# Optimization experiments

Hardware: AMD Instinct MI355X
Metric: run time of the kernel (lower is better)

## Reference

```python
import jax, jax.numpy as jnp
import numpy as np

B, C, H, W = 8, 64, 128, 128
G, DGPG = 4, 1
GD = G * DGPG          # total deformable groups = 4
COUT = 64
KH = KW = 3
K = KH * KW            # 9 kernel locations
PAD = STR = DIL = 1
HO, WO = 128, 128      # same padding, stride 1
OFFSET_SCALE = 1.0
CDG = C // GD          # channels per deformable group = 16
CPG = C // G           # input channels per conv group = 16
KOFF = 7
POFF = 3


def dwconv7(x, w, b):
    # depthwise 7x7 conv, groups == channels; w: [C,1,7,7]
    y = jax.lax.conv_general_dilated(
        x, w, window_strides=(1, 1), padding=[(POFF, POFF), (POFF, POFF)],
        feature_group_count=C, dimension_numbers=('NCHW', 'OIHW', 'NCHW'))
    return y + b[None, :, None, None]


def gn1(x, g, b):
    # GroupNorm with a single group: normalize over (C,H,W) per sample
    m = x.mean(axis=(1, 2, 3), keepdims=True)
    v = x.var(axis=(1, 2, 3), keepdims=True)
    return (x - m) * jax.lax.rsqrt(v + 1e-5) * g[None, :, None, None] + b[None, :, None, None]


def pw(x, w, b):
    # 1x1 conv; w: [O, C]
    return jnp.einsum('bchw,oc->bohw', x, w) + b[None, :, None, None]


def setup_inputs() -> dict:
    key = jax.random.key(0)
    ks = jax.random.split(key, 8)
    s = 0.02
    return {
        'x': jax.random.normal(ks[0], (B, C, H, W), jnp.float32),
        'w_dw_off': jax.random.normal(ks[1], (C, 1, KOFF, KOFF), jnp.float32) * s,
        'b_dw_off': jnp.zeros((C,), jnp.float32),
        'gn_off_g': jnp.ones((C,), jnp.float32),
        'gn_off_b': jnp.zeros((C,), jnp.float32),
        'w_pw_off': jax.random.normal(ks[2], (GD * K * 2, C), jnp.float32) * s,
        'b_pw_off': jnp.zeros((GD * K * 2,), jnp.float32),
        'w_dw_m': jax.random.normal(ks[3], (C, 1, KOFF, KOFF), jnp.float32) * s,
        'b_dw_m': jnp.zeros((C,), jnp.float32),
        'gn_m_g': jnp.ones((C,), jnp.float32),
        'gn_m_b': jnp.zeros((C,), jnp.float32),
        'w_pw_m': jax.random.normal(ks[4], (GD * K, C), jnp.float32) * s,
        'b_pw_m': jnp.zeros((GD * K,), jnp.float32),
        'weight': jax.random.normal(ks[5], (COUT, CPG, KH, KW), jnp.float32) * s,
        'bias': jax.random.normal(ks[6], (COUT,), jnp.float32) * s,
    }


def _deform_conv(x, offset, mask, weight, bias):
    # offset: [B, GD, K, 2, HO, WO] (y, x); mask: [B, GD, K, HO, WO] (softmaxed)
    ky, kx = jnp.meshgrid(jnp.arange(KH), jnp.arange(KW), indexing='ij')
    ky = ky.reshape(K).astype(x.dtype)
    kx = kx.reshape(K).astype(x.dtype)
    oy = jnp.arange(HO, dtype=x.dtype)
    ox = jnp.arange(WO, dtype=x.dtype)
    base_y = oy[None, :] * STR - PAD + ky[:, None] * DIL   # [K, HO]
    base_x = ox[None, :] * STR - PAD + kx[:, None] * DIL   # [K, WO]
    py = base_y[None, None, :, :, None] + offset[:, :, :, 0] * OFFSET_SCALE  # [B,GD,K,HO,WO]
    px = base_x[None, None, :, None, :] + offset[:, :, :, 1] * OFFSET_SCALE

    x_flat = x.reshape(B, GD, CDG, H * W)
    y0 = jnp.floor(py)
    x0 = jnp.floor(px)
    wy = py - y0
    wx = px - x0

    def gather(yi, xi):
        valid = ((yi >= 0) & (yi < H) & (xi >= 0) & (xi < W)).astype(x.dtype)
        yc = jnp.clip(yi, 0, H - 1).astype(jnp.int32)
        xc = jnp.clip(xi, 0, W - 1).astype(jnp.int32)
        idx = (yc * W + xc).reshape(B, GD, 1, K * HO * WO)
        v = jnp.take_along_axis(x_flat, idx, axis=3).reshape(B, GD, CDG, K, HO, WO)
        return v * valid[:, :, None]

    v = (gather(y0, x0) * ((1 - wy) * (1 - wx))[:, :, None]
         + gather(y0, x0 + 1) * ((1 - wy) * wx)[:, :, None]
         + gather(y0 + 1, x0) * (wy * (1 - wx))[:, :, None]
         + gather(y0 + 1, x0 + 1) * (wy * wx)[:, :, None])
    v = v * mask[:, :, None]                               # modulated samples
    v = v.reshape(B, G, CPG, K, HO, WO)
    wg = weight.reshape(G, COUT // G, CPG, K)
    out = jnp.einsum('bgckhw,gock->bgohw', v, wg).reshape(B, COUT, HO, WO)
    return out + bias[None, :, None, None]


def reference(x, w_dw_off, b_dw_off, gn_off_g, gn_off_b, w_pw_off, b_pw_off,
              w_dw_m, b_dw_m, gn_m_g, gn_m_b, w_pw_m, b_pw_m, weight, bias):
    off = pw(gn1(dwconv7(x, w_dw_off, b_dw_off), gn_off_g, gn_off_b), w_pw_off, b_pw_off)
    m = pw(gn1(dwconv7(x, w_dw_m, b_dw_m), gn_m_g, gn_m_b), w_pw_m, b_pw_m)
    offset = off.reshape(B, GD, K, 2, HO, WO)
    mask = jax.nn.softmax(m.reshape(B, GD, K, HO, WO), axis=2)  # attn over kernel points
    return _deform_conv(x, offset, mask, weight, bias)
```

## Files before the change

kernel.cpp:

```cpp
#include <hip/hip_runtime.h>
#include <hip/hip_fp16.h>
#include <math.h>

#define HW     16384
#define IMG_H  128
#define IMG_W  128

typedef _Float16 f16x2 __attribute__((ext_vector_type(2)));
typedef __fp16 fp16v2 __attribute__((ext_vector_type(2)));
typedef _Float16 f16x4 __attribute__((ext_vector_type(4)));
typedef float f32x4 __attribute__((ext_vector_type(4)));

#define OFF_T2    ((size_t)0)
#define OFF_XT    ((size_t)8388608)
#define OFF_WT    ((size_t)12582912)
#define OFF_PART  ((size_t)12599040)
#define OFF_AD    ((size_t)12631808)
#define OFF_WB    ((size_t)19711744)
#define OFF_WDW2  ((size_t)19716352)
#define OFF_WBO   ((size_t)19719936)
#define OFF_WBM   ((size_t)19752704)
#define OFF_DC    ((size_t)19769088)

__global__ void k_prep(const float* __restrict__ wpw_off,
                       const float* __restrict__ wpw_m,
                       const float* __restrict__ wdef,
                       const float* __restrict__ wdwo,
                       const float* __restrict__ wdwm,
                       float* __restrict__ ws) {
    int i = blockIdx.x * 256 + threadIdx.x;
    if (i < 6912) {
        int c = i / 108, o = i % 108;
        ws[OFF_WT + i] = (o < 72) ? wpw_off[o * 64 + c] : wpw_m[(o - 72) * 64 + c];
    } else if (i < 9216) {
        int j = i - 6912;
        int lane = j & 63;
        int gt = j >> 6;
        int tap = gt % 9, g = gt / 9;
        int oc = lane & 15, qh = lane >> 4;
        union { ushort h[4]; uint2 u; } pk;
#pragma unroll
        for (int jj = 0; jj < 4; ++jj) {
            float wv = wdef[((g * 16 + oc) * 16 + (4 * qh + jj)) * 9 + tap];
            pk.h[jj] = __half_as_ushort(__float2half(wv));
        }
        ((uint2*)(ws + OFF_WB))[j] = pk.u;
    } else if (i < 12800) {
        int j = i - 9216;
        int q = j & 3;
        int r = j >> 2;
        int dy = r % 7;
        int cv = (r / 7) & 1;
        int c = r / 14;
        const float* src = cv ? wdwm : wdwo;
        int dx0 = q * 2;
        float w0 = src[c * 49 + dy * 7 + dx0];
        float w1 = (dx0 + 1 < 7) ? src[c * 49 + dy * 7 + dx0 + 1] : 0.f;
        union { __half h[2]; uint u; } pk;
        pk.h[0] = __float2half(w0);
        pk.h[1] = __float2half(w1);
        ((uint*)(ws + OFF_WDW2))[j] = pk.u;
    }
}

__global__ __launch_bounds__(256) void k_trans(const float* __restrict__ x,
                                               __half* __restrict__ xT) {
    int n = blockIdx.x * 256 + threadIdx.x;
    int p = n & (HW - 1);
    int bg = n >> 14;
    const float* src = x + (size_t)bg * 16 * HW + p;
    union { __half2 h2[8]; uint4 u[2]; } pk;
#pragma unroll
    for (int i = 0; i < 8; ++i) {
        float a = src[(size_t)(2 * i) * HW];
        float bq = src[(size_t)(2 * i + 1) * HW];
        pk.h2[i] = __halves2half2(__float2half(a), __float2half(bq));
    }
    uint4* dst = (uint4*)(xT + (size_t)n * 16);
    dst[0] = pk.u[0];
    dst[1] = pk.u[1];
}

__global__ __launch_bounds__(256) void k_dw(const float* __restrict__ x,
                                            const float* __restrict__ bdwo,
                                            const float* __restrict__ bdwm,
                                            const uint* __restrict__ wdw2,
                                            uint2* __restrict__ t2p,
                                            float* __restrict__ partial) {
    int bid = blockIdx.x;
    int b = bid >> 9;
    int c2 = (bid >> 4) & 31;
    int stripe = (bid & 15) * 8;
    int t = threadIdx.x;
    int cb = t & 31;
    int row = stripe + (t >> 5);
    int c0 = c2 * 2;

    float vo[2][4], vm[2][4];
    float s1o = 0.f, s2o = 0.f, s1m = 0.f, s2m = 0.f;
    union CV { fp16v2 v; f16x2 h; };
    union WU { uint u; f16x2 h; };

#pragma unroll
    for (int ch = 0; ch < 2; ++ch) {
        int c = c0 + ch;
        const float4* pl = (const float4*)(x + ((size_t)(b * 64 + c)) * HW);
        const uint* wp = wdw2 + c * 56;
        float acco[4] = {0.f, 0.f, 0.f, 0.f};
        float accm[4] = {0.f, 0.f, 0.f, 0.f};
#pragma unroll
        for (int dy = 0; dy < 7; ++dy) {
            int iy = row - 3 + dy;
            if (iy >= 0 && iy < IMG_H) {
                const float4* prow = pl + iy * 32;
                float4 f4 = prow[cb];
                float4 f4m = prow[cb == 0 ? 0 : cb - 1];
                float4 f4p = prow[cb == 31 ? 31 : cb + 1];
                bool le = (cb == 0), re = (cb == 31);
                float v[11];
                v[0] = le ? 0.f : f4m.y;
                v[1] = le ? 0.f : f4m.z;
                v[2] = le ? 0.f : f4m.w;
                v[3] = f4.x; v[4] = f4.y; v[5] = f4.z; v[6] = f4.w;
                v[7] = re ? 0.f : f4p.x;
                v[8] = re ? 0.f : f4p.y;
                v[9] = re ? 0.f : f4p.z;
                v[10] = re ? 0.f : f4p.w;
                f16x2 hp[10];
#pragma unroll
                for (int d = 0; d < 10; ++d) {
                    CV cv;
                    cv.v = __builtin_amdgcn_cvt_pkrtz(v[d], v[d + 1]);
                    hp[d] = cv.h;
                }
#pragma unroll
                for (int cc = 0; cc < 4; ++cc) {
                    WU w0, w1, w2, w3, u0, u1, u2, u3;
                    w0.u = wp[dy * 4 + 0]; w1.u = wp[dy * 4 + 1];
                    w2.u = wp[dy * 4 + 2]; w3.u = wp[dy * 4 + 3];
                    u0.u = wp[28 + dy * 4 + 0]; u1.u = wp[28 + dy * 4 + 1];
                    u2.u = wp[28 + dy * 4 + 2]; u3.u = wp[28 + dy * 4 + 3];
                    float ao = acco[cc], am = accm[cc];
                    ao = __builtin_amdgcn_fdot2(hp[cc],     w0.h, ao, false);
                    ao = __builtin_amdgcn_fdot2(hp[cc + 2], w1.h, ao, false);
                    ao = __builtin_amdgcn_fdot2(hp[cc + 4], w2.h, ao, false);
                    ao = __builtin_amdgcn_fdot2(hp[cc + 6], w3.h, ao, false);
                    am = __builtin_amdgcn_fdot2(hp[cc],     u0.h, am, false);
                    am = __builtin_amdgcn_fdot2(hp[cc + 2], u1.h, am, false);
                    am = __builtin_amdgcn_fdot2(hp[cc + 4], u2.h, am, false);
                    am = __builtin_amdgcn_fdot2(hp[cc + 6], u3.h, am, false);
                    acco[cc] = ao; accm[cc] = am;
                }
            }
        }
        float bo = bdwo[c], bm = bdwm[c];
#pragma unroll
        for (int cc = 0; cc < 4; ++cc) {
            float o_ = acco[cc] + bo, m_ = accm[cc] + bm;
            vo[ch][cc] = o_; vm[ch][cc] = m_;
            s1o += o_; s2o += o_ * o_; s1m += m_; s2m += m_ * m_;
        }
    }

    union { uint2 u2[4]; uint4 u4[2]; } ot;
#pragma unroll
    for (int cc = 0; cc < 4; ++cc) {
        ot.u2[cc].x = (uint)__half_as_ushort(__float2half(vo[0][cc])) |
                      ((uint)__half_as_ushort(__float2half(vo[1][cc])) << 16);
        ot.u2[cc].y = (uint)__half_as_ushort(__float2half(vm[0][cc])) |
                      ((uint)__half_as_ushort(__float2half(vm[1][cc])) << 16);
    }
    uint4* dst = (uint4*)(t2p + ((size_t)(b * 32 + c2) * HW + row * IMG_W + cb * 4));
    dst[0] = ot.u4[0];
    dst[1] = ot.u4[1];

#pragma unroll
    for (int d = 32; d; d >>= 1) {
        s1o += __shfl_down(s1o, d);
        s2o += __shfl_down(s2o, d);
        s1m += __shfl_down(s1m, d);
        s2m += __shfl_down(s2m, d);
    }
    __shared__ float red[4][4];
    if ((t & 63) == 0) {
        int w = t >> 6;
        red[w][0] = s1o; red[w][1] = s2o; red[w][2] = s1m; red[w][3] = s2m;
    }
    __syncthreads();
    if (t < 4) {
        float v = red[0][t] + red[1][t] + red[2][t] + red[3][t];
        partial[(size_t)bid * 4 + t] = v;
    }
}

__global__ __launch_bounds__(256) void k_fin(const float* __restrict__ partial,
                      const float* __restrict__ gog, const float* __restrict__ gob,
                      const float* __restrict__ gmg, const float* __restrict__ gmb,
                      float* __restrict__ ad) {
    int b = blockIdx.x, t = threadIdx.x;
    const float4* pp = (const float4*)partial + (size_t)b * 512;
    float4 s = make_float4(0.f, 0.f, 0.f, 0.f);
#pragma unroll
    for (int i = 0; i < 2; ++i) {
        float4 v = pp[t + i * 256];
        s.x += v.x; s.y += v.y; s.z += v.z; s.w += v.w;
    }
#pragma unroll
    for (int d = 32; d; d >>= 1) {
        s.x += __shfl_down(s.x, d);
        s.y += __shfl_down(s.y, d);
        s.z += __shfl_down(s.z, d);
        s.w += __shfl_down(s.w, d);
    }
    __shared__ float red[4][4];
    if ((t & 63) == 0) {
        int w = t >> 6;
        red[w][0] = s.x; red[w][1] = s.y; red[w][2] = s.z; red[w][3] = s.w;
    }
    __syncthreads();
    if (t < 64) {
        float s1o = red[0][0] + red[1][0] + red[2][0] + red[3][0];
        float s2o = red[0][1] + red[1][1] + red[2][1] + red[3][1];
        float s1m = red[0][2] + red[1][2] + red[2][2] + red[3][2];
        float s2m = red[0][3] + red[1][3] + red[2][3] + red[3][3];
        int c = t;
        const float invN = 1.f / 1048576.f;
        float m_o = s1o * invN;
        float v_o = s2o * invN - m_o * m_o;
        float i_o = rsqrtf(v_o + 1e-5f);
        float m_m = s1m * invN;
        float v_m = s2m * invN - m_m * m_m;
        float i_m = rsqrtf(v_m + 1e-5f);
        float a_o = i_o * gog[c];
        float d_o = gob[c] - m_o * a_o;
        float a_m = i_m * gmg[c];
        float d_m = gmb[c] - m_m * a_m;
        ((float4*)ad)[b * 64 + c] = make_float4(a_o, d_o, a_m, d_m);
    }
}

__global__ __launch_bounds__(256) void k_fold(const float* __restrict__ wT,
                                              const float* __restrict__ ad,
                                              const float* __restrict__ bpo,
                                              const float* __restrict__ bpm,
                                              uint2* __restrict__ wbo,
                                              uint2* __restrict__ wbm,
                                              float* __restrict__ dconst) {
    int b = blockIdx.x, t = threadIdx.x;
    const float* adb = ad + b * 256;
    for (int i = t; i < 2048; i += 256) {
        int lane = i & 63;
        int f = i >> 6;
        int g = f >> 3, kk = (f >> 1) & 3, nf = f & 1;
        int n = lane & 15, q = lane >> 4;
        int out = nf * 16 + n;
        union { ushort h[4]; uint2 u; } pk;
#pragma unroll
        for (int jj = 0; jj < 4; ++jj) {
            int ch = kk * 16 + 4 * q + jj;
            float w = (out < 18) ? adb[ch * 4 + 0] * wT[ch * 108 + g * 18 + out] : 0.f;
            pk.h[jj] = __half_as_ushort(__float2half(w));
        }
        wbo[((size_t)(b * 4) + g) * 8 * 64 + (size_t)(kk * 2 + nf) * 64 + lane] = pk.u;
    }
    for (int i = t; i < 1024; i += 256) {
        int lane = i & 63;
        int f = i >> 6;
        int g = f >> 2, kk = f & 3;
        int n = lane & 15, q = lane >> 4;
        union { ushort h[4]; uint2 u; } pk;
#pragma unroll
        for (int jj = 0; jj < 4; ++jj) {
            int ch = kk * 16 + 4 * q + jj;
            float w = (n < 9) ? adb[ch * 4 + 2] * wT[ch * 108 + 72 + g * 9 + n] : 0.f;
            pk.h[jj] = __half_as_ushort(__float2half(w));
        }
        wbm[((size_t)(b * 4) + g) * 4 * 64 + (size_t)kk * 64 + lane] = pk.u;
    }
    if (t < 108) {
        float s = (t < 72) ? bpo[t] : bpm[t - 72];
        for (int c = 0; c < 64; ++c) {
            float d = (t < 72) ? adb[c * 4 + 1] : adb[c * 4 + 3];
            s = fmaf(d, wT[c * 108 + t], s);
        }
        dconst[b * 108 + t] = s;
    }
}

__global__ __launch_bounds__(256, 4) void k_gthf(const uint2* __restrict__ t2p,
                                                 const uint2* __restrict__ wbo,
                                                 const uint2* __restrict__ wbm,
                                                 const float* __restrict__ dconst,
                                                 const __half* __restrict__ xT,
                                                 const uint2* __restrict__ wb,
                                                 const float* __restrict__ bias,
                                                 float* __restrict__ out) {
    __shared__ union SMem {
        struct {
            uint4 xsA[506];
            uint4 xsB[506];
            uint  slab[5120];
        } s;
        float shout[4864];
    } sm;

    int tid = threadIdx.x;
    int bid = blockIdx.x;
    int bg = bid >> 6;
    int tile = bid & 63;
    int tr = tile >> 3, tc = tile & 7;
    int r0 = tr * 16, c0 = tc * 16;
    int g = bg & 3, b = bg >> 2;
    int wr0 = r0 - 3, wc0 = c0 - 3;

    const __half* xg = xT + (size_t)bg * HW * 16;

#pragma unroll
    for (int it = 0; it < 2; ++it) {
        int idx = tid + it * 256;
        if (idx < 484) {
            int ly = idx / 22, lx = idx - ly * 22;
            int sr = wr0 + ly; sr = sr < 0 ? 0 : (sr > 127 ? 127 : sr);
            int sc = wc0 + lx; sc = sc < 0 ? 0 : (sc > 127 ? 127 : sc);
            const uint4* src = (const uint4*)(xg + (size_t)(sr * IMG_W + sc) * 16);
            sm.s.xsA[ly * 23 + lx] = src[0];
            sm.s.xsB[ly * 23 + lx] = src[1];
        }
    }

    int row = r0 + (tid >> 4), col = c0 + (tid & 15);
    int p = row * IMG_W + col;
    int lane = tid & 63, wv = tid >> 6;
    int m_idx = lane & 15, q_idx = lane >> 4;

    union BU { uint2 u; f16x4 h; };

    const uint2* wboP = wbo + ((size_t)(b * 4) + g) * 8 * 64 + lane;
    const uint2* wbmP = wbm + ((size_t)(b * 4) + g) * 4 * 64 + lane;
    f16x4 bO[8], bM[4];
#pragma unroll
    for (int i = 0; i < 8; ++i) { BU t; t.u = wboP[i * 64]; bO[i] = t.h; }
#pragma unroll
    for (int i = 0; i < 4; ++i) { BU t; t.u = wbmP[i * 64]; bM[i] = t.h; }

    const uint2* wbp = wb + (size_t)(g * 9) * 64 + lane;
    f16x4 bfr[9];
#pragma unroll
    for (int k = 0; k < 9; ++k) { BU t; t.u = wbp[k * 64]; bfr[k] = t.h; }

    uint* aslab = sm.s.slab + wv * 1280;
    const uint2* tp = t2p + (size_t)b * 32 * HW + p;

    f32x4 accO0[4], accO1[4], accM[4];
#pragma unroll
    for (int s = 0; s < 4; ++s) {
        accO0[s] = (f32x4){0.f, 0.f, 0.f, 0.f};
        accO1[s] = (f32x4){0.f, 0.f, 0.f, 0.f};
        accM[s]  = (f32x4){0.f, 0.f, 0.f, 0.f};
    }

#pragma unroll
    for (int kk = 0; kk < 4; ++kk) {
        uint2 v[8];
#pragma unroll
        for (int j = 0; j < 8; ++j) v[j] = tp[(size_t)(kk * 8 + j) * HW];
        uint* rowp = aslab + lane * 20;
        ((uint4*)rowp)[0] = make_uint4(v[0].x, v[1].x, v[2].x, v[3].x);
        ((uint4*)rowp)[1] = make_uint4(v[4].x, v[5].x, v[6].x, v[7].x);
        ((uint4*)(rowp + 8))[0] = make_uint4(v[0].y, v[1].y, v[2].y, v[3].y);
        ((uint4*)(rowp + 8))[1] = make_uint4(v[4].y, v[5].y, v[6].y, v[7].y);
#pragma unroll
        for (int s = 0; s < 4; ++s) {
            const uint* pr = aslab + (s * 16 + m_idx) * 20 + 2 * q_idx;
            BU ao, am;
            ao.u = *(const uint2*)pr;
            am.u = *(const uint2*)(pr + 8);
            accO0[s] = __builtin_amdgcn_mfma_f32_16x16x16f16(ao.h, bO[kk * 2 + 0], accO0[s], 0, 0, 0);
            accO1[s] = __builtin_amdgcn_mfma_f32_16x16x16f16(ao.h, bO[kk * 2 + 1], accO1[s], 0, 0, 0);
            accM[s]  = __builtin_amdgcn_mfma_f32_16x16x16f16(am.h, bM[kk], accM[s], 0, 0, 0);
        }
    }

    const float* dc = dconst + b * 108;

#pragma unroll
    for (int s = 0; s < 4; ++s)
#pragma unroll
        for (int j = 0; j < 4; ++j) {
            int px = s * 16 + 4 * q_idx + j;
            union { __half2 h2; uint u; } pk;
            pk.h2 = __halves2half2(__float2half(accO0[s][j]),
                                   __float2half(accO1[s][j]));
            aslab[px * 20 + m_idx] = pk.u;
        }
    float facc[18];
    {
        const uint4* dr = (const uint4*)(aslab + lane * 20);
        uint4 d0 = dr[0], d1 = dr[1], d2 = dr[2], d3 = dr[3];
        uint du[16] = {d0.x, d0.y, d0.z, d0.w, d1.x, d1.y, d1.z, d1.w,
                       d2.x, d2.y, d2.z, d2.w, d3.x, d3.y, d3.z, d3.w};
        union { uint u; __half2 h2; } cv;
#pragma unroll
        for (int i = 0; i < 16; ++i) {
            cv.u = du[i];
            float2 f = __half22float2(cv.h2);
            facc[i] = f.x + dc[g * 18 + i];
            if (i < 2) facc[16 + i] = f.y + dc[g * 18 + 16 + i];
        }
    }

    {
        float* fsl = (float*)aslab;
#pragma unroll
        for (int s = 0; s < 4; ++s)
#pragma unroll
            for (int j = 0; j < 4; ++j) {
                int px = s * 16 + 4 * q_idx + j;
                fsl[px * 20 + m_idx] = accM[s][j];
            }
        float macc[9];
#pragma unroll
        for (int k = 0; k < 9; ++k) macc[k] = fsl[lane * 20 + k] + dc[72 + g * 9 + k];
        float mx = macc[0];
#pragma unroll
        for (int k = 1; k < 9; ++k) mx = fmaxf(mx, macc[k]);
        float ssum = 0.f;
#pragma unroll
        for (int k = 0; k < 9; ++k) {
            float e = __expf(macc[k] - mx);
            macc[k] = e;
            ssum += e;
        }
        float inv = 1.f / ssum;
#pragma unroll
        for (int k = 0; k < 9; ++k) facc[k] = facc[k], macc[k] *= inv;

        __syncthreads();

        uint4* shvw = (uint4*)aslab + lane * 3;
        const _Float16* shvh = (const _Float16*)aslab;

        f32x4 acc[4];
#pragma unroll
        for (int s = 0; s < 4; ++s) acc[s] = (f32x4){0.f, 0.f, 0.f, 0.f};

#pragma unroll
        for (int k = 0; k < 9; ++k) {
            float mk = macc[k];
            float py = (float)(row + k / 3 - 1) + facc[k * 2 + 0];
            float px = (float)(col + k % 3 - 1) + facc[k * 2 + 1];
            float y0f = floorf(py), x0f = floorf(px);
            float wy = py - y0f, wx = px - x0f;
            int iy0 = (int)y0f, ix0 = (int)x0f;
            int iy1 = iy0 + 1, ix1 = ix0 + 1;
            float fy0 = (iy0 >= 0 && iy0 < IMG_H) ? (1.f - wy) : 0.f;
            float fy1 = (iy1 >= 0 && iy1 < IMG_H) ? wy : 0.f;
            float fx0 = (ix0 >= 0 && ix0 < IMG_W) ? (1.f - wx) : 0.f;
            float fx1 = (ix1 >= 0 && ix1 < IMG_W) ? wx : 0.f;
            __half2 f00h = __float2half2_rn(fy0 * fx0 * mk);
            __half2 f01h = __float2half2_rn(fy0 * fx1 * mk);
            __half2 f10h = __float2half2_rn(fy1 * fx0 * mk);
            __half2 f11h = __float2half2_rn(fy1 * fx1 * mk);
            int ly0 = iy0 - wr0; ly0 = ly0 < 0 ? 0 : (ly0 > 21 ? 21 : ly0);
            int ly1 = iy1 - wr0; ly1 = ly1 < 0 ? 0 : (ly1 > 21 ? 21 : ly1);
            int lx0 = ix0 - wc0; lx0 = lx0 < 0 ? 0 : (lx0 > 21 ? 21 : lx0);
            int lx1 = ix1 - wc0; lx1 = lx1 < 0 ? 0 : (lx1 > 21 ? 21 : lx1);
            int i00 = ly0 * 23 + lx0, i01 = ly0 * 23 + lx1;
            int i10 = ly1 * 23 + lx0, i11 = ly1 * 23 + lx1;
            union Q8 { uint4 u[2]; __half2 h2[8]; };
            Q8 q00, q01, q10, q11;
            q00.u[0] = sm.s.xsA[i00]; q00.u[1] = sm.s.xsB[i00];
            q01.u[0] = sm.s.xsA[i01]; q01.u[1] = sm.s.xsB[i01];
            q10.u[0] = sm.s.xsA[i10]; q10.u[1] = sm.s.xsB[i10];
            q11.u[0] = sm.s.xsA[i11]; q11.u[1] = sm.s.xsB[i11];
            union V8 { __half2 h2[4]; uint4 u; };
            V8 pa, pb;
#pragma unroll
            for (int i = 0; i < 4; ++i) {
                __half2 vh = __hmul2(f00h, q00.h2[i]);
                vh = __hfma2(f01h, q01.h2[i], vh);
                vh = __hfma2(f10h, q10.h2[i], vh);
                vh = __hfma2(f11h, q11.h2[i], vh);
                pa.h2[i] = vh;
            }
#pragma unroll
            for (int i = 4; i < 8; ++i) {
                __half2 vh = __hmul2(f00h, q00.h2[i]);
                vh = __hfma2(f01h, q01.h2[i], vh);
                vh = __hfma2(f10h, q10.h2[i], vh);
                vh = __hfma2(f11h, q11.h2[i], vh);
                pb.h2[i - 4] = vh;
            }
            shvw[0] = pa.u;
            shvw[1] = pb.u;
#pragma unroll
            for (int s = 0; s < 4; ++s) {
                f16x4 af = *(const f16x4*)(shvh +
                            ((size_t)(s * 16 + m_idx)) * 24 + q_idx * 4);
                acc[s] = __builtin_amdgcn_mfma_f32_16x16x16f16(af, bfr[k], acc[s], 0, 0, 0);
            }
        }

        __syncthreads();

#pragma unroll
        for (int s = 0; s < 4; ++s)
#pragma unroll
            for (int j = 0; j < 4; ++j)
                sm.shout[(wv * 64 + s * 16 + 4 * q_idx + j) * 19 + m_idx] = acc[s][j];

        float* outp = out + ((size_t)b * 64 + g * 16) * HW + p;
#pragma unroll
        for (int o = 0; o < 16; ++o)
            outp[(size_t)o * HW] = sm.shout[tid * 19 + o] + bias[g * 16 + o];
    }
}

extern "C" void kernel_launch(void* const* d_in, const int* in_sizes, int n_in,
                              void* d_out, int out_size, void* d_ws, size_t ws_size,
                              hipStream_t stream) {
    const float* x        = (const float*)d_in[0];
    const float* w_dw_off = (const float*)d_in[1];
    const float* b_dw_off = (const float*)d_in[2];
    const float* gn_off_g = (const float*)d_in[3];
    const float* gn_off_b = (const float*)d_in[4];
    const float* w_pw_off = (const float*)d_in[5];
    const float* b_pw_off = (const float*)d_in[6];
    const float* w_dw_m   = (const float*)d_in[7];
    const float* b_dw_m   = (const float*)d_in[8];
    const float* gn_m_g   = (const float*)d_in[9];
    const float* gn_m_b   = (const float*)d_in[10];
    const float* w_pw_m   = (const float*)d_in[11];
    const float* b_pw_m   = (const float*)d_in[12];
    const float* weight   = (const float*)d_in[13];
    const float* bias     = (const float*)d_in[14];

    float* ws = (float*)d_ws;
    uint2* t2p    = (uint2*)(ws + OFF_T2);
    __half* xT    = (__half*)(ws + OFF_XT);
    float* wT     = ws + OFF_WT;
    float* part   = ws + OFF_PART;
    float* adb    = ws + OFF_AD;
    const uint2* wb = (const uint2*)(ws + OFF_WB);
    const uint* wdw2 = (const uint*)(ws + OFF_WDW2);
    uint2* wbo    = (uint2*)(ws + OFF_WBO);
    uint2* wbm    = (uint2*)(ws + OFF_WBM);
    float* dconst = ws + OFF_DC;

    k_prep<<<50, 256, 0, stream>>>(w_pw_off, w_pw_m, weight, w_dw_off, w_dw_m, ws);
    k_trans<<<2048, 256, 0, stream>>>(x, xT);
    k_dw<<<4096, 256, 0, stream>>>(x, b_dw_off, b_dw_m, wdw2, t2p, part);
    k_fin<<<8, 256, 0, stream>>>(part, gn_off_g, gn_off_b, gn_m_g, gn_m_b, adb);
    k_fold<<<8, 256, 0, stream>>>(wT, adb, b_pw_off, b_pw_m, wbo, wbm, dconst);
    k_gthf<<<2048, 256, 0, stream>>>(t2p, wbo, wbm, dconst, xT, wb, bias, (float*)d_out);
}
```

Before: 100.7 us.

## Fuse GN finalize with weight folding and software-pipeline loads in gather kernel

Merges the GroupNorm finalize and weight-fold kernels into one launch that keeps the per-channel scale and shift in shared memory, removing a launch and a global round trip. In the main gather kernel, the x-tile loads are held in registers and written to shared memory only after the offset/mask MFMA stage, so their latency overlaps that compute. The t2p feature loads are double-buffered across kk iterations, and the deform-conv weight fragment loads are moved later in the kernel. Holding more values in registers raises register pressure, which may reduce occupancy under the 256x4 launch bounds.

```diff
diff --git a/kernel.cpp b/kernel.cpp
--- a/kernel.cpp
+++ b/kernel.cpp
@@ -15,7 +15,6 @@
 #define OFF_XT    ((size_t)8388608)
 #define OFF_WT    ((size_t)12582912)
 #define OFF_PART  ((size_t)12599040)
-#define OFF_AD    ((size_t)12631808)
 #define OFF_WB    ((size_t)19711744)
 #define OFF_WDW2  ((size_t)19716352)
 #define OFF_WBO   ((size_t)19719936)
@@ -193,61 +192,58 @@
     }
 }
 
-__global__ __launch_bounds__(256) void k_fin(const float* __restrict__ partial,
+__global__ __launch_bounds__(256) void k_finfold(const float* __restrict__ partial,
                       const float* __restrict__ gog, const float* __restrict__ gob,
                       const float* __restrict__ gmg, const float* __restrict__ gmb,
-                      float* __restrict__ ad) {
+                      const float* __restrict__ wT,
+                      const float* __restrict__ bpo,
+                      const float* __restrict__ bpm,
+                      uint2* __restrict__ wbo,
+                      uint2* __restrict__ wbm,
+                      float* __restrict__ dconst) {
+    __shared__ float adsh[256];
     int b = blockIdx.x, t = threadIdx.x;
-    const float4* pp = (const float4*)partial + (size_t)b * 512;
-    float4 s = make_float4(0.f, 0.f, 0.f, 0.f);
-#pragma unroll
-    for (int i = 0; i < 2; ++i) {
-        float4 v = pp[t + i * 256];
-        s.x += v.x; s.y += v.y; s.z += v.z; s.w += v.w;
-    }
-#pragma unroll
-    for (int d = 32; d; d >>= 1) {
-        s.x += __shfl_down(s.x, d);
-        s.y += __shfl_down(s.y, d);
-        s.z += __shfl_down(s.z, d);
-        s.w += __shfl_down(s.w, d);
-    }
-    __shared__ float red[4][4];
-    if ((t & 63) == 0) {
-        int w = t >> 6;
-        red[w][0] = s.x; red[w][1] = s.y; red[w][2] = s.z; red[w][3] = s.w;
-    }
-    __syncthreads();
-    if (t < 64) {
-        float s1o = red[0][0] + red[1][0] + red[2][0] + red[3][0];
-        float s2o = red[0][1] + red[1][1] + red[2][1] + red[3][1];
-        float s1m = red[0][2] + red[1][2] + red[2][2] + red[3][2];
-        float s2m = red[0][3] + red[1][3] + red[2][3] + red[3][3];
-        int c = t;
-        const float invN = 1.f / 1048576.f;
-        float m_o = s1o * invN;
-        float v_o = s2o * invN - m_o * m_o;
-        float i_o = rsqrtf(v_o + 1e-5f);
-        float m_m = s1m * invN;
-        float v_m = s2m * invN - m_m * m_m;
-        float i_m = rsqrtf(v_m + 1e-5f);
-        float a_o = i_o * gog[c];
-        float d_o = gob[c] - m_o * a_o;
-        float a_m = i_m * gmg[c];
-        float d_m = gmb[c] - m_m * a_m;
-        ((float4*)ad)[b * 64 + c] = make_float4(a_o, d_o, a_m, d_m);
-    }
-}
-
-__global__ __launch_bounds__(256) void k_fold(const float* __restrict__ wT,
-                                              const float* __restrict__ ad,
-                                              const float* __restrict__ bpo,
-                                              const float* __restrict__ bpm,
-                                              uint2* __restrict__ wbo,
-                                              uint2* __restrict__ wbm,
-                                              float* __restrict__ dconst) {
-    int b = blockIdx.x, t = threadIdx.x;
-    const float* adb = ad + b * 256;
+    {
+        const float4* pp = (const float4*)partial + (size_t)b * 512;
+        float4 s = make_float4(0.f, 0.f, 0.f, 0.f);
+#pragma unroll
+        for (int i = 0; i < 2; ++i) {
+            float4 v = pp[t + i * 256];
+            s.x += v.x; s.y += v.y; s.z += v.z; s.w += v.w;
+        }
+#pragma unroll
+        for (int d = 32; d; d >>= 1) {
+            s.x += __shfl_down(s.x, d);
+            s.y += __shfl_down(s.y, d);
+            s.z += __shfl_down(s.z, d);
+            s.w += __shfl_down(s.w, d);
+        }
+        __shared__ float red[4][4];
+        if ((t & 63) == 0) {
+            int w = t >> 6;
+            red[w][0] = s.x; red[w][1] = s.y; red[w][2] = s.z; red[w][3] = s.w;
+        }
+        __syncthreads();
+        if (t < 64) {
+            float s1o = red[0][0] + red[1][0] + red[2][0] + red[3][0];
+            float s2o = red[0][1] + red[1][1] + red[2][1] + red[3][1];
+            float s1m = red[0][2] + red[1][2] + red[2][2] + red[3][2];
+            float s2m = red[0][3] + red[1][3] + red[2][3] + red[3][3];
+            int c = t;
+            const float invN = 1.f / 1048576.f;
+            float m_o = s1o * invN;
+            float v_o = s2o * invN - m_o * m_o;
+            float i_o = rsqrtf(v_o + 1e-5f);
+            float m_m = s1m * invN;
+            float v_m = s2m * invN - m_m * m_m;
+            float i_m = rsqrtf(v_m + 1e-5f);
+            adsh[c * 4 + 0] = i_o * gog[c];
+            adsh[c * 4 + 1] = gob[c] - m_o * (i_o * gog[c]);
+            adsh[c * 4 + 2] = i_m * gmg[c];
+            adsh[c * 4 + 3] = gmb[c] - m_m * (i_m * gmg[c]);
+        }
+        __syncthreads();
+    }
     for (int i = t; i < 2048; i += 256) {
         int lane = i & 63;
         int f = i >> 6;
@@ -258,7 +254,7 @@
 #pragma unroll
         for (int jj = 0; jj < 4; ++jj) {
             int ch = kk * 16 + 4 * q + jj;
-            float w = (out < 18) ? adb[ch * 4 + 0] * wT[ch * 108 + g * 18 + out] : 0.f;
+            float w = (out < 18) ? adsh[ch * 4 + 0] * wT[ch * 108 + g * 18 + out] : 0.f;
             pk.h[jj] = __half_as_ushort(__float2half(w));
         }
         wbo[((size_t)(b * 4) + g) * 8 * 64 + (size_t)(kk * 2 + nf) * 64 + lane] = pk.u;
@@ -272,7 +268,7 @@
 #pragma unroll
         for (int jj = 0; jj < 4; ++jj) {
             int ch = kk * 16 + 4 * q + jj;
-            float w = (n < 9) ? adb[ch * 4 + 2] * wT[ch * 108 + 72 + g * 9 + n] : 0.f;
+            float w = (n < 9) ? adsh[ch * 4 + 2] * wT[ch * 108 + 72 + g * 9 + n] : 0.f;
             pk.h[jj] = __half_as_ushort(__float2half(w));
         }
         wbm[((size_t)(b * 4) + g) * 4 * 64 + (size_t)kk * 64 + lane] = pk.u;
@@ -280,7 +276,7 @@
     if (t < 108) {
         float s = (t < 72) ? bpo[t] : bpm[t - 72];
         for (int c = 0; c < 64; ++c) {
-            float d = (t < 72) ? adb[c * 4 + 1] : adb[c * 4 + 3];
+            float d = (t < 72) ? adsh[c * 4 + 1] : adsh[c * 4 + 3];
             s = fmaf(d, wT[c * 108 + t], s);
         }
         dconst[b * 108 + t] = s;
@@ -315,16 +311,20 @@
 
     const __half* xg = xT + (size_t)bg * HW * 16;
 
+    int sidx[2];
+    uint4 sA[2], sB[2];
 #pragma unroll
     for (int it = 0; it < 2; ++it) {
         int idx = tid + it * 256;
+        sidx[it] = -1;
         if (idx < 484) {
             int ly = idx / 22, lx = idx - ly * 22;
             int sr = wr0 + ly; sr = sr < 0 ? 0 : (sr > 127 ? 127 : sr);
             int sc = wc0 + lx; sc = sc < 0 ? 0 : (sc > 127 ? 127 : sc);
             const uint4* src = (const uint4*)(xg + (size_t)(sr * IMG_W + sc) * 16);
-            sm.s.xsA[ly * 23 + lx] = src[0];
-            sm.s.xsB[ly * 23 + lx] = src[1];
+            sA[it] = src[0];
+            sB[it] = src[1];
+            sidx[it] = ly * 23 + lx;
         }
     }
 
@@ -343,11 +343,6 @@
 #pragma unroll
     for (int i = 0; i < 4; ++i) { BU t; t.u = wbmP[i * 64]; bM[i] = t.h; }
 
-    const uint2* wbp = wb + (size_t)(g * 9) * 64 + lane;
-    f16x4 bfr[9];
-#pragma unroll
-    for (int k = 0; k < 9; ++k) { BU t; t.u = wbp[k * 64]; bfr[k] = t.h; }
-
     uint* aslab = sm.s.slab + wv * 1280;
     const uint2* tp = t2p + (size_t)b * 32 * HW + p;
 
@@ -359,16 +354,21 @@
         accM[s]  = (f32x4){0.f, 0.f, 0.f, 0.f};
     }
 
+    uint2 cur[8], nxt[8];
+#pragma unroll
+    for (int j = 0; j < 8; ++j) cur[j] = tp[(size_t)j * HW];
+
 #pragma unroll
     for (int kk = 0; kk < 4; ++kk) {
-        uint2 v[8];
-#pragma unroll
-        for (int j = 0; j < 8; ++j) v[j] = tp[(size_t)(kk * 8 + j) * HW];
+        if (kk < 3) {
+#pragma unroll
+            for (int j = 0; j < 8; ++j) nxt[j] = tp[(size_t)((kk + 1) * 8 + j) * HW];
+        }
         uint* rowp = aslab + lane * 20;
-        ((uint4*)rowp)[0] = make_uint4(v[0].x, v[1].x, v[2].x, v[3].x);
-        ((uint4*)rowp)[1] = make_uint4(v[4].x, v[5].x, v[6].x, v[7].x);
-        ((uint4*)(rowp + 8))[0] = make_uint4(v[0].y, v[1].y, v[2].y, v[3].y);
-        ((uint4*)(rowp + 8))[1] = make_uint4(v[4].y, v[5].y, v[6].y, v[7].y);
+        ((uint4*)rowp)[0] = make_uint4(cur[0].x, cur[1].x, cur[2].x, cur[3].x);
+        ((uint4*)rowp)[1] = make_uint4(cur[4].x, cur[5].x, cur[6].x, cur[7].x);
+        ((uint4*)(rowp + 8))[0] = make_uint4(cur[0].y, cur[1].y, cur[2].y, cur[3].y);
+        ((uint4*)(rowp + 8))[1] = make_uint4(cur[4].y, cur[5].y, cur[6].y, cur[7].y);
 #pragma unroll
         for (int s = 0; s < 4; ++s) {
             const uint* pr = aslab + (s * 16 + m_idx) * 20 + 2 * q_idx;
@@ -379,7 +379,16 @@
             accO1[s] = __builtin_amdgcn_mfma_f32_16x16x16f16(ao.h, bO[kk * 2 + 1], accO1[s], 0, 0, 0);
             accM[s]  = __builtin_amdgcn_mfma_f32_16x16x16f16(am.h, bM[kk], accM[s], 0, 0, 0);
         }
-    }
+#pragma unroll
+        for (int j = 0; j < 8; ++j) cur[j] = nxt[j];
+    }
+
+#pragma unroll
+    for (int it = 0; it < 2; ++it)
+        if (sidx[it] >= 0) {
+            sm.s.xsA[sidx[it]] = sA[it];
+            sm.s.xsB[sidx[it]] = sB[it];
+        }
 
     const float* dc = dconst + b * 108;
 
@@ -409,6 +418,7 @@
         }
     }
 
+    float macc[9];
     {
         float* fsl = (float*)aslab;
 #pragma unroll
@@ -418,7 +428,6 @@
                 int px = s * 16 + 4 * q_idx + j;
                 fsl[px * 20 + m_idx] = accM[s][j];
             }
-        float macc[9];
 #pragma unroll
         for (int k = 0; k < 9; ++k) macc[k] = fsl[lane * 20 + k] + dc[72 + g * 9 + k];
         float mx = macc[0];
@@ -433,87 +442,92 @@
         }
         float inv = 1.f / ssum;
 #pragma unroll
-        for (int k = 0; k < 9; ++k) facc[k] = facc[k], macc[k] *= inv;
-
-        __syncthreads();
-
-        uint4* shvw = (uint4*)aslab + lane * 3;
-        const _Float16* shvh = (const _Float16*)aslab;
-
-        f32x4 acc[4];
-#pragma unroll
-        for (int s = 0; s < 4; ++s) acc[s] = (f32x4){0.f, 0.f, 0.f, 0.f};
-
-#pragma unroll
-        for (int k = 0; k < 9; ++k) {
-            float mk = macc[k];
-            float py = (float)(row + k / 3 - 1) + facc[k * 2 + 0];
-            float px = (float)(col + k % 3 - 1) + facc[k * 2 + 1];
-            float y0f = floorf(py), x0f = floorf(px);
-            float wy = py - y0f, wx = px - x0f;
-            int iy0 = (int)y0f, ix0 = (int)x0f;
-            int iy1 = iy0 + 1, ix1 = ix0 + 1;
-            float fy0 = (iy0 >= 0 && iy0 < IMG_H) ? (1.f - wy) : 0.f;
-            float fy1 = (iy1 >= 0 && iy1 < IMG_H) ? wy : 0.f;
-            float fx0 = (ix0 >= 0 && ix0 < IMG_W) ? (1.f - wx) : 0.f;
-            float fx1 = (ix1 >= 0 && ix1 < IMG_W) ? wx : 0.f;
-            __half2 f00h = __float2half2_rn(fy0 * fx0 * mk);
-            __half2 f01h = __float2half2_rn(fy0 * fx1 * mk);
-            __half2 f10h = __float2half2_rn(fy1 * fx0 * mk);
-            __half2 f11h = __float2half2_rn(fy1 * fx1 * mk);
-            int ly0 = iy0 - wr0; ly0 = ly0 < 0 ? 0 : (ly0 > 21 ? 21 : ly0);
-            int ly1 = iy1 - wr0; ly1 = ly1 < 0 ? 0 : (ly1 > 21 ? 21 : ly1);
-            int lx0 = ix0 - wc0; lx0 = lx0 < 0 ? 0 : (lx0 > 21 ? 21 : lx0);
-            int lx1 = ix1 - wc0; lx1 = lx1 < 0 ? 0 : (lx1 > 21 ? 21 : lx1);
-            int i00 = ly0 * 23 + lx0, i01 = ly0 * 23 + lx1;
-            int i10 = ly1 * 23 + lx0, i11 = ly1 * 23 + lx1;
-            union Q8 { uint4 u[2]; __half2 h2[8]; };
-            Q8 q00, q01, q10, q11;
-            q00.u[0] = sm.s.xsA[i00]; q00.u[1] = sm.s.xsB[i00];
-            q01.u[0] = sm.s.xsA[i01]; q01.u[1] = sm.s.xsB[i01];
-            q10.u[0] = sm.s.xsA[i10]; q10.u[1] = sm.s.xsB[i10];
-            q11.u[0] = sm.s.xsA[i11]; q11.u[1] = sm.s.xsB[i11];
-            union V8 { __half2 h2[4]; uint4 u; };
-            V8 pa, pb;
-#pragma unroll
-            for (int i = 0; i < 4; ++i) {
-                __half2 vh = __hmul2(f00h, q00.h2[i]);
-                vh = __hfma2(f01h, q01.h2[i], vh);
-                vh = __hfma2(f10h, q10.h2[i], vh);
-                vh = __hfma2(f11h, q11.h2[i], vh);
-                pa.h2[i] = vh;
-            }
-#pragma unroll
-            for (int i = 4; i < 8; ++i) {
-                __half2 vh = __hmul2(f00h, q00.h2[i]);
-                vh = __hfma2(f01h, q01.h2[i], vh);
-                vh = __hfma2(f10h, q10.h2[i], vh);
-                vh = __hfma2(f11h, q11.h2[i], vh);
-                pb.h2[i - 4] = vh;
-            }
-            shvw[0] = pa.u;
-            shvw[1] = pb.u;
-#pragma unroll
-            for (int s = 0; s < 4; ++s) {
-                f16x4 af = *(const f16x4*)(shvh +
-                            ((size_t)(s * 16 + m_idx)) * 24 + q_idx * 4);
-                acc[s] = __builtin_amdgcn_mfma_f32_16x16x16f16(af, bfr[k], acc[s], 0, 0, 0);
-            }
-        }
-
-        __syncthreads();
-
-#pragma unroll
-        for (int s = 0; s < 4; ++s)
-#pragma unroll
-            for (int j = 0; j < 4; ++j)
-                sm.shout[(wv * 64 + s * 16 + 4 * q_idx + j) * 19 + m_idx] = acc[s][j];
-
-        float* outp = out + ((size_t)b * 64 + g * 16) * HW + p;
-#pragma unroll
-        for (int o = 0; o < 16; ++o)
-            outp[(size_t)o * HW] = sm.shout[tid * 19 + o] + bias[g * 16 + o];
-    }
+        for (int k = 0; k < 9; ++k) macc[k] *= inv;
+    }
+
+    const uint2* wbp = wb + (size_t)(g * 9) * 64 + lane;
+    f16x4 bfr[9];
+#pragma unroll
+    for (int k = 0; k < 9; ++k) { BU t; t.u = wbp[k * 64]; bfr[k] = t.h; }
+
+    __syncthreads();
+
+    uint4* shvw = (uint4*)aslab + lane * 3;
+    const _Float16* shvh = (const _Float16*)aslab;
+
+    f32x4 acc[4];
+#pragma unroll
+    for (int s = 0; s < 4; ++s) acc[s] = (f32x4){0.f, 0.f, 0.f, 0.f};
+
+#pragma unroll
+    for (int k = 0; k < 9; ++k) {
+        float mk = macc[k];
+        float py = (float)(row + k / 3 - 1) + facc[k * 2 + 0];
+        float px = (float)(col + k % 3 - 1) + facc[k * 2 + 1];
+        float y0f = floorf(py), x0f = floorf(px);
+        float wy = py - y0f, wx = px - x0f;
+        int iy0 = (int)y0f, ix0 = (int)x0f;
+        int iy1 = iy0 + 1, ix1 = ix0 + 1;
+        float fy0 = (iy0 >= 0 && iy0 < IMG_H) ? (1.f - wy) : 0.f;
+        float fy1 = (iy1 >= 0 && iy1 < IMG_H) ? wy : 0.f;
+        float fx0 = (ix0 >= 0 && ix0 < IMG_W) ? (1.f - wx) : 0.f;
+        float fx1 = (ix1 >= 0 && ix1 < IMG_W) ? wx : 0.f;
+        __half2 f00h = __float2half2_rn(fy0 * fx0 * mk);
+        __half2 f01h = __float2half2_rn(fy0 * fx1 * mk);
+        __half2 f10h = __float2half2_rn(fy1 * fx0 * mk);
+        __half2 f11h = __float2half2_rn(fy1 * fx1 * mk);
+        int ly0 = iy0 - wr0; ly0 = ly0 < 0 ? 0 : (ly0 > 21 ? 21 : ly0);
+        int ly1 = iy1 - wr0; ly1 = ly1 < 0 ? 0 : (ly1 > 21 ? 21 : ly1);
+        int lx0 = ix0 - wc0; lx0 = lx0 < 0 ? 0 : (lx0 > 21 ? 21 : lx0);
+        int lx1 = ix1 - wc0; lx1 = lx1 < 0 ? 0 : (lx1 > 21 ? 21 : lx1);
+        int i00 = ly0 * 23 + lx0, i01 = ly0 * 23 + lx1;
+        int i10 = ly1 * 23 + lx0, i11 = ly1 * 23 + lx1;
+        union Q8 { uint4 u[2]; __half2 h2[8]; };
+        Q8 q00, q01, q10, q11;
+        q00.u[0] = sm.s.xsA[i00]; q00.u[1] = sm.s.xsB[i00];
+        q01.u[0] = sm.s.xsA[i01]; q01.u[1] = sm.s.xsB[i01];
+        q10.u[0] = sm.s.xsA[i10]; q10.u[1] = sm.s.xsB[i10];
+        q11.u[0] = sm.s.xsA[i11]; q11.u[1] = sm.s.xsB[i11];
+        union V8 { __half2 h2[4]; uint4 u; };
+        V8 pa, pb;
+#pragma unroll
+        for (int i = 0; i < 4; ++i) {
+            __half2 vh = __hmul2(f00h, q00.h2[i]);
+            vh = __hfma2(f01h, q01.h2[i], vh);
+            vh = __hfma2(f10h, q10.h2[i], vh);
+            vh = __hfma2(f11h, q11.h2[i], vh);
+            pa.h2[i] = vh;
+        }
+#pragma unroll
+        for (int i = 4; i < 8; ++i) {
+            __half2 vh = __hmul2(f00h, q00.h2[i]);
+            vh = __hfma2(f01h, q01.h2[i], vh);
+            vh = __hfma2(f10h, q10.h2[i], vh);
+            vh = __hfma2(f11h, q11.h2[i], vh);
+            pb.h2[i - 4] = vh;
+        }
+        shvw[0] = pa.u;
+        shvw[1] = pb.u;
+#pragma unroll
+        for (int s = 0; s < 4; ++s) {
+            f16x4 af = *(const f16x4*)(shvh +
+                        ((size_t)(s * 16 + m_idx)) * 24 + q_idx * 4);
+            acc[s] = __builtin_amdgcn_mfma_f32_16x16x16f16(af, bfr[k], acc[s], 0, 0, 0);
+        }
+    }
+
+    __syncthreads();
+
+#pragma unroll
+    for (int s = 0; s < 4; ++s)
+#pragma unroll
+        for (int j = 0; j < 4; ++j)
+            sm.shout[(wv * 64 + s * 16 + 4 * q_idx + j) * 19 + m_idx] = acc[s][j];
+
+    float* outp = out + ((size_t)b * 64 + g * 16) * HW + p;
+#pragma unroll
+    for (int o = 0; o < 16; ++o)
+        outp[(size_t)o * HW] = sm.shout[tid * 19 + o] + bias[g * 16 + o];
 }
 
 extern "C" void kernel_launch(void* const* d_in, const int* in_sizes, int n_in,
@@ -540,7 +554,6 @@
     __half* xT    = (__half*)(ws + OFF_XT);
     float* wT     = ws + OFF_WT;
     float* part   = ws + OFF_PART;
-    float* adb    = ws + OFF_AD;
     const uint2* wb = (const uint2*)(ws + OFF_WB);
     const uint* wdw2 = (const uint*)(ws + OFF_WDW2);
     uint2* wbo    = (uint2*)(ws + OFF_WBO);
@@ -550,7 +563,7 @@
     k_prep<<<50, 256, 0, stream>>>(w_pw_off, w_pw_m, weight, w_dw_off, w_dw_m, ws);
     k_trans<<<2048, 256, 0, stream>>>(x, xT);
     k_dw<<<4096, 256, 0, stream>>>(x, b_dw_off, b_dw_m, wdw2, t2p, part);
-    k_fin<<<8, 256, 0, stream>>>(part, gn_off_g, gn_off_b, gn_m_g, gn_m_b, adb);
-    k_fold<<<8, 256, 0, stream>>>(wT, adb, b_pw_off, b_pw_m, wbo, wbm, dconst);
+    k_finfold<<<8, 256, 0, stream>>>(part, gn_off_g, gn_off_b, gn_m_g, gn_m_b,
+                                     wT, b_pw_off, b_pw_m, wbo, wbm, dconst);
     k_gthf<<<2048, 256, 0, stream>>>(t2p, wbo, wbm, dconst, xT, wb, bias, (float*)d_out);
 }
```

Measured after the change: 103.7 us. 1.03x slower.
